# Kernel optimization log

Hardware: AMD Instinct MI355X
Metric: run time of the kernel (lower is better)

Reference implementation:

```python
import jax, jax.numpy as jnp
import numpy as np

B, P, L = 32, 16, 512
VOCAB, D = 50000, 256  # embed_dim == hidden_dim (required for attn_type='dot')
SCALE, PAGE_SCALE = 10.0, 10.0


def sparsemax(z):
    # z: [..., K]; sort-based sparsemax (Martins & Astudillo 2016)
    K = z.shape[-1]
    zs = jnp.sort(z, axis=-1)[..., ::-1]            # descending
    k = jnp.arange(1, K + 1, dtype=z.dtype)
    cs = jnp.cumsum(zs, axis=-1)
    support = 1.0 + k * zs > cs                     # [..., K] bool
    kmax = jnp.sum(support, axis=-1, keepdims=True) # support size (>=1)
    cs_k = jnp.take_along_axis(cs, kmax.astype(jnp.int32) - 1, axis=-1)
    tau = (cs_k - 1.0) / kmax.astype(z.dtype)
    return jnp.maximum(z - tau, 0.0)


def setup_inputs() -> dict:
    key = jax.random.key(0)
    k1, k2, k3, k4, k5, k6, k7 = jax.random.split(key, 7)
    seq_ids = jax.random.randint(k1, (B, P, L), 0, VOCAB)
    num_pages = jax.random.randint(k2, (B,), 1, P + 1)        # 1..P valid pages
    seq_lengths = jax.random.randint(k3, (B, P), 1, L + 1)    # 1..L valid tokens
    emb_table = jax.random.uniform(k4, (VOCAB, D), jnp.float32, -0.1, 0.1)
    V = jax.random.normal(k5, (D, 1), jnp.float32)
    W = jax.random.normal(k6, (D, 1), jnp.float32)
    dec_w = jax.random.normal(k7, (1, D), jnp.float32) * 0.05  # decoder, no bias
    return {"seq_ids": seq_ids, "num_pages": num_pages, "seq_lengths": seq_lengths,
            "emb_table": emb_table, "V": V, "W": W, "dec_w": dec_w}


def reference(seq_ids, num_pages, seq_lengths, emb_table, V, W, dec_w):
    # Embedding lookup (dropout is identity in eval mode)
    hidden_vecs = emb_table[seq_ids]                         # [B,P,L,D]
    # Word-level scores (attn_type='dot': inter_out = hidden_vecs)
    scores = jnp.einsum('bpld,do->bpl', hidden_vecs, V) / SCALE  # [B,P,L]
    # Ragged word mask: original double loop only masks pages j < num_pages[i]
    pos = jnp.arange(L)[None, None, :]                       # [1,1,L]
    page_idx = jnp.arange(P)[None, :, None]                  # [1,P,1]
    word_mask = (pos >= seq_lengths[:, :, None]) & (page_idx < num_pages[:, None, None])
    scores = jnp.where(word_mask, -999.0, scores)
    attn = jax.nn.softmax(scores, axis=-1)[:, :, None, :]    # [B,P,1,L]
    webpage_vec = jnp.einsum('bpl,bpld->bpd', attn[:, :, 0, :], hidden_vecs)  # [B,P,D]
    # Page-level scores + sparsemax over pages
    page_scores = jnp.einsum('bpd,do->bp', webpage_vec, W) / PAGE_SCALE
    page_mask = jnp.arange(P)[None, :] >= num_pages[:, None]
    page_scores = jnp.where(page_mask, -9999.0, page_scores)
    page_attn = sparsemax(page_scores)[:, None, :]           # [B,1,P]
    final_vec = jnp.einsum('bp,bpd->bd', page_attn[:, 0, :], webpage_vec)  # [B,D]
    senti_scores = final_vec @ dec_w.T                       # [B,1]
    probs = jax.nn.sigmoid(senti_scores)
    return (probs, senti_scores, attn, page_attn, final_vec, page_scores, webpage_vec)
```

## Files before the change

### kernel.cpp

```cpp
#include <hip/hip_runtime.h>
#include <math.h>

constexpr int Bn = 32, Pn = 16, Ln = 512, Dn = 256, VOC = 50000;

__global__ __launch_bounds__(256) void k_embdot(const float* __restrict__ emb,
                                               const float* __restrict__ V,
                                               const float* __restrict__ W,
                                               float2* __restrict__ eVW,
                                               ushort* __restrict__ bt)
{
    int row  = blockIdx.x * 4 + (threadIdx.x >> 6);
    if (row >= VOC) return;
    int lane = threadIdx.x & 63;
    float4 r  = ((const float4*)(emb + (size_t)row * Dn))[lane];
    float4 v  = ((const float4*)V)[lane];
    float4 w  = ((const float4*)W)[lane];

    uint u0 = __float_as_uint(r.x), u1 = __float_as_uint(r.y),
         u2 = __float_as_uint(r.z), u3 = __float_as_uint(r.w);
    ushort4 h;
    h.x = (ushort)((u0 + 0x7fffu + ((u0 >> 16) & 1u)) >> 16);
    h.y = (ushort)((u1 + 0x7fffu + ((u1 >> 16) & 1u)) >> 16);
    h.z = (ushort)((u2 + 0x7fffu + ((u2 >> 16) & 1u)) >> 16);
    h.w = (ushort)((u3 + 0x7fffu + ((u3 >> 16) & 1u)) >> 16);
    *(ushort4*)(bt + (size_t)row * Dn + lane * 4) = h;

    float dv = r.x*v.x + r.y*v.y + r.z*v.z + r.w*v.w;
    float dw = r.x*w.x + r.y*w.y + r.z*w.z + r.w*w.w;
#pragma unroll
    for (int o = 32; o; o >>= 1) { dv += __shfl_xor(dv, o); dw += __shfl_xor(dw, o); }
    if (lane == 0) eVW[row] = make_float2(dv / 10.0f, dw / 10.0f);
}

__global__ __launch_bounds__(512) void k_page(const int* __restrict__ seq_ids,
                                              const int* __restrict__ num_pages,
                                              const int* __restrict__ seq_lengths,
                                              const ushort* __restrict__ bt,
                                              const float2* __restrict__ eVW,
                                              float* __restrict__ attn_out,
                                              float* __restrict__ pscore_out,
                                              float* __restrict__ web_out)
{
    int bp = blockIdx.x;
    int b  = bp >> 4, p = bp & 15;
    int tid = threadIdx.x, lane = tid & 63, wv = tid >> 6;

    __shared__ int   ids[Ln];
    __shared__ float sc[Ln];
    __shared__ float redm[8], reds[8], redp[8];
    __shared__ float part[16][Dn];

    const int* sid = seq_ids + (size_t)bp * Ln;
    int  slen = seq_lengths[bp];
    bool vp   = (p < num_pages[b]);
    int  Lv   = vp ? slen : Ln;

    int id = sid[tid];
    ids[tid] = id;
    float2 vw = eVW[id];
    float wreg = vw.y;
    sc[tid] = (vp && tid >= slen) ? -999.0f : vw.x;
    __syncthreads();

    float mx = sc[tid];
#pragma unroll
    for (int o = 32; o; o >>= 1) mx = fmaxf(mx, __shfl_xor(mx, o));
    if (lane == 0) redm[wv] = mx;
    __syncthreads();
    mx = redm[0];
#pragma unroll
    for (int w = 1; w < 8; ++w) mx = fmaxf(mx, redm[w]);

    float e = expf(sc[tid] - mx);
    sc[tid] = e;
    float pw = e * wreg;
    float sum = e, ps = pw;
#pragma unroll
    for (int o = 32; o; o >>= 1) { sum += __shfl_xor(sum, o); ps += __shfl_xor(ps, o); }
    if (lane == 0) { reds[wv] = sum; redp[wv] = ps; }
    __syncthreads();
    sum = 0.f; ps = 0.f;
#pragma unroll
    for (int w = 0; w < 8; ++w) { sum += reds[w]; ps += redp[w]; }
    float inv = 1.0f / sum;

    attn_out[(size_t)bp * Ln + tid] = sc[tid] * inv;
    if (tid == 0) pscore_out[bp] = vp ? ps * inv : -9999.0f;

    int s  = 2 * wv + (lane >> 5);
    int cl = lane & 31;
    float a0=0.f,a1=0.f,a2=0.f,a3=0.f,a4=0.f,a5=0.f,a6=0.f,a7=0.f;
#pragma unroll 4
    for (int l = s; l < Lv; l += 16) {
        float wgt = sc[l];
        uint4 q = *(const uint4*)(bt + (size_t)ids[l] * Dn + cl * 8);
        a0 += wgt * __uint_as_float(q.x << 16);
        a1 += wgt * __uint_as_float(q.x & 0xffff0000u);
        a2 += wgt * __uint_as_float(q.y << 16);
        a3 += wgt * __uint_as_float(q.y & 0xffff0000u);
        a4 += wgt * __uint_as_float(q.z << 16);
        a5 += wgt * __uint_as_float(q.z & 0xffff0000u);
        a6 += wgt * __uint_as_float(q.w << 16);
        a7 += wgt * __uint_as_float(q.w & 0xffff0000u);
    }
    float4 lo = make_float4(a0*inv, a1*inv, a2*inv, a3*inv);
    float4 hi = make_float4(a4*inv, a5*inv, a6*inv, a7*inv);
    ((float4*)&part[s][cl * 8])[0] = lo;
    ((float4*)&part[s][cl * 8])[1] = hi;
    __syncthreads();

    if (tid < Dn) {
        float acc = 0.f;
#pragma unroll
        for (int w = 0; w < 16; ++w) acc += part[w][tid];
        web_out[(size_t)bp * Dn + tid] = acc;
    }
}

__global__ __launch_bounds__(256) void k_final(const float* __restrict__ dec_w,
                                               const float* __restrict__ pscore,
                                               const float* __restrict__ web,
                                               float* __restrict__ probs,
                                               float* __restrict__ senti,
                                               float* __restrict__ pattn,
                                               float* __restrict__ fvec)
{
    int b = blockIdx.x, tid = threadIdx.x, lane = tid & 63, wv = tid >> 6;
    __shared__ float pa[Pn];
    __shared__ float red[4];

    if (tid == 0) {
        float z[Pn], zs[Pn], csum[Pn];
        for (int i = 0; i < Pn; ++i) { z[i] = pscore[b * Pn + i]; zs[i] = z[i]; }
        for (int i = 1; i < Pn; ++i) {
            float key = zs[i]; int j = i - 1;
            while (j >= 0 && zs[j] < key) { zs[j + 1] = zs[j]; --j; }
            zs[j + 1] = key;
        }
        int kmax = 0; float cs = 0.f;
        for (int k = 0; k < Pn; ++k) {
            cs += zs[k];
            csum[k] = cs;
            if (1.0f + (float)(k + 1) * zs[k] > cs) kmax = k + 1;
        }
        float tau = (csum[kmax - 1] - 1.0f) / (float)kmax;
        for (int i = 0; i < Pn; ++i) pa[i] = fmaxf(z[i] - tau, 0.0f);
    }
    __syncthreads();

    float fv = 0.f;
#pragma unroll
    for (int p = 0; p < Pn; ++p) fv += pa[p] * web[((size_t)b * Pn + p) * Dn + tid];
    fvec[(size_t)b * Dn + tid] = fv;
    if (tid < Pn) pattn[b * Pn + tid] = pa[tid];

    float t = fv * dec_w[tid];
#pragma unroll
    for (int o = 32; o; o >>= 1) t += __shfl_xor(t, o);
    if (lane == 0) red[wv] = t;
    __syncthreads();
    if (tid == 0) {
        float s = red[0] + red[1] + red[2] + red[3];
        senti[b] = s;
        probs[b] = 1.0f / (1.0f + expf(-s));
    }
}

extern "C" void kernel_launch(void* const* d_in, const int* in_sizes, int n_in,
                              void* d_out, int out_size, void* d_ws, size_t ws_size,
                              hipStream_t stream) {
    const int*   seq_ids     = (const int*)d_in[0];
    const int*   num_pages   = (const int*)d_in[1];
    const int*   seq_lengths = (const int*)d_in[2];
    const float* emb         = (const float*)d_in[3];
    const float* V           = (const float*)d_in[4];
    const float* W           = (const float*)d_in[5];
    const float* dec_w       = (const float*)d_in[6];

    float* out    = (float*)d_out;
    float* probs  = out;
    float* senti  = probs + Bn;
    float* attn   = senti + Bn;
    float* pattn  = attn  + (size_t)Bn * Pn * Ln;
    float* fvec   = pattn + Bn * Pn;
    float* pscore = fvec  + (size_t)Bn * Dn;
    float* web    = pscore + Bn * Pn;

    float2* eVW = (float2*)d_ws;
    ushort* bt  = (ushort*)((char*)d_ws + (size_t)VOC * sizeof(float2));

    k_embdot<<<(VOC + 3) / 4, 256, 0, stream>>>(emb, V, W, eVW, bt);
    k_page<<<Bn * Pn, 512, 0, stream>>>(seq_ids, num_pages, seq_lengths,
                                        bt, eVW, attn, pscore, web);
    k_final<<<Bn, 256, 0, stream>>>(dec_w, pscore, web, probs, senti, pattn, fvec);
}
```

Baseline: 39.24 us.

## Slice bf16 table by column and split page kernel into score and gather

The bf16 embedding copy is stored as 8 column slices of 32 values each, and the per-page kernel is split in two. A score kernel computes the softmax and page score. A new gather kernel launches one 64-thread block per page and column slice, reads the ids and attention weights back from global memory, and reduces across lanes with shuffles. The goal is more parallelism and better L2 locality, since each slice is about 3.2MB, at the cost of an extra launch, a global round-trip for attn, and reloading the ids eight times.

```diff
diff --git a/kernel.cpp b/kernel.cpp
--- a/kernel.cpp
+++ b/kernel.cpp
@@ -2,12 +2,13 @@
 #include <math.h>
 
 constexpr int Bn = 32, Pn = 16, Ln = 512, Dn = 256, VOC = 50000;
+constexpr int NSL = 8, SLC = 32;
 
 __global__ __launch_bounds__(256) void k_embdot(const float* __restrict__ emb,
                                                const float* __restrict__ V,
                                                const float* __restrict__ W,
                                                float2* __restrict__ eVW,
-                                               ushort* __restrict__ bt)
+                                               ushort* __restrict__ bts)
 {
     int row  = blockIdx.x * 4 + (threadIdx.x >> 6);
     if (row >= VOC) return;
@@ -23,7 +24,8 @@
     h.y = (ushort)((u1 + 0x7fffu + ((u1 >> 16) & 1u)) >> 16);
     h.z = (ushort)((u2 + 0x7fffu + ((u2 >> 16) & 1u)) >> 16);
     h.w = (ushort)((u3 + 0x7fffu + ((u3 >> 16) & 1u)) >> 16);
-    *(ushort4*)(bt + (size_t)row * Dn + lane * 4) = h;
+    size_t off = (size_t)(lane >> 3) * VOC * SLC + (size_t)row * SLC + (lane & 7) * 4;
+    *(ushort4*)(bts + off) = h;
 
     float dv = r.x*v.x + r.y*v.y + r.z*v.z + r.w*v.w;
     float dw = r.x*w.x + r.y*w.y + r.z*w.z + r.w*w.w;
@@ -32,31 +34,24 @@
     if (lane == 0) eVW[row] = make_float2(dv / 10.0f, dw / 10.0f);
 }
 
-__global__ __launch_bounds__(512) void k_page(const int* __restrict__ seq_ids,
-                                              const int* __restrict__ num_pages,
-                                              const int* __restrict__ seq_lengths,
-                                              const ushort* __restrict__ bt,
-                                              const float2* __restrict__ eVW,
-                                              float* __restrict__ attn_out,
-                                              float* __restrict__ pscore_out,
-                                              float* __restrict__ web_out)
+__global__ __launch_bounds__(512) void k_score(const int* __restrict__ seq_ids,
+                                               const int* __restrict__ num_pages,
+                                               const int* __restrict__ seq_lengths,
+                                               const float2* __restrict__ eVW,
+                                               float* __restrict__ attn_out,
+                                               float* __restrict__ pscore_out)
 {
     int bp = blockIdx.x;
     int b  = bp >> 4, p = bp & 15;
     int tid = threadIdx.x, lane = tid & 63, wv = tid >> 6;
 
-    __shared__ int   ids[Ln];
     __shared__ float sc[Ln];
     __shared__ float redm[8], reds[8], redp[8];
-    __shared__ float part[16][Dn];
-
-    const int* sid = seq_ids + (size_t)bp * Ln;
+
     int  slen = seq_lengths[bp];
     bool vp   = (p < num_pages[b]);
-    int  Lv   = vp ? slen : Ln;
-
-    int id = sid[tid];
-    ids[tid] = id;
+
+    int id = seq_ids[(size_t)bp * Ln + tid];
     float2 vw = eVW[id];
     float wreg = vw.y;
     sc[tid] = (vp && tid >= slen) ? -999.0f : vw.x;
@@ -72,7 +67,6 @@
     for (int w = 1; w < 8; ++w) mx = fmaxf(mx, redm[w]);
 
     float e = expf(sc[tid] - mx);
-    sc[tid] = e;
     float pw = e * wreg;
     float sum = e, ps = pw;
 #pragma unroll
@@ -84,16 +78,44 @@
     for (int w = 0; w < 8; ++w) { sum += reds[w]; ps += redp[w]; }
     float inv = 1.0f / sum;
 
-    attn_out[(size_t)bp * Ln + tid] = sc[tid] * inv;
+    attn_out[(size_t)bp * Ln + tid] = e * inv;
     if (tid == 0) pscore_out[bp] = vp ? ps * inv : -9999.0f;
-
-    int s  = 2 * wv + (lane >> 5);
-    int cl = lane & 31;
+}
+
+__global__ __launch_bounds__(64) void k_gather(const int* __restrict__ seq_ids,
+                                               const int* __restrict__ num_pages,
+                                               const int* __restrict__ seq_lengths,
+                                               const ushort* __restrict__ bts,
+                                               const float* __restrict__ attn,
+                                               float* __restrict__ web)
+{
+    int blk = blockIdx.x;
+    int s  = blk & 7, bp = blk >> 3;
+    int b  = bp >> 4, p  = bp & 15;
+    int lane = threadIdx.x;
+
+    int  slen = seq_lengths[bp];
+    int  Lv   = (p < num_pages[b]) ? slen : Ln;
+
+    __shared__ int   ids[Ln];
+    __shared__ float w[Ln];
+
+    const int4*   sid4 = (const int4*)(seq_ids + (size_t)bp * Ln);
+    const float4* at4  = (const float4*)(attn + (size_t)bp * Ln);
+    for (int i = lane; i < Ln / 4; i += 64) {
+        ((int4*)ids)[i] = sid4[i];
+        ((float4*)w)[i] = at4[i];
+    }
+    __syncthreads();
+
+    const ushort* base = bts + (size_t)s * VOC * SLC;
+    int rg = lane >> 2;
+    int cg = lane & 3;
     float a0=0.f,a1=0.f,a2=0.f,a3=0.f,a4=0.f,a5=0.f,a6=0.f,a7=0.f;
 #pragma unroll 4
-    for (int l = s; l < Lv; l += 16) {
-        float wgt = sc[l];
-        uint4 q = *(const uint4*)(bt + (size_t)ids[l] * Dn + cl * 8);
+    for (int l = rg; l < Lv; l += 16) {
+        float wgt = w[l];
+        uint4 q = *(const uint4*)(base + (size_t)ids[l] * SLC + cg * 8);
         a0 += wgt * __uint_as_float(q.x << 16);
         a1 += wgt * __uint_as_float(q.x & 0xffff0000u);
         a2 += wgt * __uint_as_float(q.y << 16);
@@ -103,17 +125,17 @@
         a6 += wgt * __uint_as_float(q.w << 16);
         a7 += wgt * __uint_as_float(q.w & 0xffff0000u);
     }
-    float4 lo = make_float4(a0*inv, a1*inv, a2*inv, a3*inv);
-    float4 hi = make_float4(a4*inv, a5*inv, a6*inv, a7*inv);
-    ((float4*)&part[s][cl * 8])[0] = lo;
-    ((float4*)&part[s][cl * 8])[1] = hi;
-    __syncthreads();
-
-    if (tid < Dn) {
-        float acc = 0.f;
-#pragma unroll
-        for (int w = 0; w < 16; ++w) acc += part[w][tid];
-        web_out[(size_t)bp * Dn + tid] = acc;
+#pragma unroll
+    for (int o = 4; o <= 32; o <<= 1) {
+        a0 += __shfl_xor(a0, o); a1 += __shfl_xor(a1, o);
+        a2 += __shfl_xor(a2, o); a3 += __shfl_xor(a3, o);
+        a4 += __shfl_xor(a4, o); a5 += __shfl_xor(a5, o);
+        a6 += __shfl_xor(a6, o); a7 += __shfl_xor(a7, o);
+    }
+    if (rg == 0) {
+        float* dst = web + (size_t)bp * Dn + s * SLC + cg * 8;
+        ((float4*)dst)[0] = make_float4(a0, a1, a2, a3);
+        ((float4*)dst)[1] = make_float4(a4, a5, a6, a7);
     }
 }
 
@@ -187,10 +209,12 @@
     float* web    = pscore + Bn * Pn;
 
     float2* eVW = (float2*)d_ws;
-    ushort* bt  = (ushort*)((char*)d_ws + (size_t)VOC * sizeof(float2));
-
-    k_embdot<<<(VOC + 3) / 4, 256, 0, stream>>>(emb, V, W, eVW, bt);
-    k_page<<<Bn * Pn, 512, 0, stream>>>(seq_ids, num_pages, seq_lengths,
-                                        bt, eVW, attn, pscore, web);
-    k_final<<<Bn, 256, 0, stream>>>(dec_w, pscore, web, probs, senti, pattn, fvec);
-}
+    ushort* bts = (ushort*)((char*)d_ws + (size_t)VOC * sizeof(float2));
+
+    k_embdot<<<(VOC + 3) / 4, 256, 0, stream>>>(emb, V, W, eVW, bts);
+    k_score <<<Bn * Pn, 512, 0, stream>>>(seq_ids, num_pages, seq_lengths,
+                                          eVW, attn, pscore);
+    k_gather<<<Bn * Pn * NSL, 64, 0, stream>>>(seq_ids, num_pages, seq_lengths,
+                                               bts, attn, web);
+    k_final <<<Bn, 256, 0, stream>>>(dec_w, pscore, web, probs, senti, pattn, fvec);
+}
```

Measured after the change: 41.31 us. 5.3% more time.
